# Kernel optimization log

Hardware: AMD Instinct MI355X
Metric: run time of the kernel (lower is better)

## Reference

```python
import jax, jax.numpy as jnp
import numpy as np

AVG_STEP_WEIGHTING = 0.002


def _mean_rbf_kernel(a, b):
    """Mean over all (i,j) of exp(-||a_i - b_j||^2 / 2), features flattened.

    Equivalent to the original per-row loop: (1/N) * sum_i mean_j k(b, a_i).
    Uses the Gram trick to avoid materializing (N, M, D) intermediates.
    """
    A = a.reshape(a.shape[0], -1)  # (N, D)
    B = b.reshape(b.shape[0], -1)  # (M, D)
    sq_a = jnp.sum(A * A, axis=1)  # (N,)
    sq_b = jnp.sum(B * B, axis=1)  # (M,)
    # (N, M) pairwise squared distances; clamp tiny negatives from fp error
    d2 = jnp.maximum(sq_a[:, None] + sq_b[None, :] - 2.0 * (A @ B.T), 0.0)
    return jnp.mean(jnp.exp(-0.5 * d2))


def setup_inputs() -> dict:
    key = jax.random.key(0)
    kx, ky = jax.random.split(key)
    N, M, D1, D2 = 4096, 4096, 24, 8
    x = jax.random.normal(kx, (N, D1, D2), dtype=jnp.float32)
    y = jax.random.normal(ky, (M, D1, D2), dtype=jnp.float32)
    avg_step = jnp.asarray(5.0, dtype=jnp.float32)
    return {"x": x, "y": y, "avg_step": avg_step}


def reference(x, y, avg_step):
    XX = _mean_rbf_kernel(x, x)
    XY = _mean_rbf_kernel(x, y)
    YY = _mean_rbf_kernel(y, y)
    mmd = XX + YY - 2.0 * XY
    loss = mmd + (jnp.maximum(jnp.asarray(1.0, x.dtype), avg_step) - 1.0) * AVG_STEP_WEIGHTING
    return (loss, mmd)
```

## Files before the change

kernel.cpp:

```cpp
#include <hip/hip_runtime.h>
#include <hip/hip_bf16.h>

typedef __attribute__((ext_vector_type(8))) short short8;
typedef __attribute__((ext_vector_type(4))) float float4v;

#define N_ROWS 4096
#define K_DIM  192
#define TILE   128
#define NT     32
#define NSYM   528
#define NBLK   2080
#define LDSS   104
#define C1     (-0.72134752044448179f)
#define LOG2E  (1.4426950408889634f)

__global__ void prep_kernel(const float* __restrict__ x, const float* __restrict__ y,
                            __hip_bfloat16* __restrict__ xb, __hip_bfloat16* __restrict__ yb,
                            float* __restrict__ sqx, float* __restrict__ sqy)
{
    int w    = (blockIdx.x * blockDim.x + threadIdx.x) >> 6;
    int lane = threadIdx.x & 63;
    if (w >= 2 * N_ROWS) return;
    const float*      src = (w < N_ROWS) ? (x + (size_t)w * K_DIM) : (y + (size_t)(w - N_ROWS) * K_DIM);
    __hip_bfloat16*   dst = (w < N_ROWS) ? (xb + (size_t)w * K_DIM) : (yb + (size_t)(w - N_ROWS) * K_DIM);
    float s = 0.f;
    #pragma unroll
    for (int i = 0; i < 3; ++i) {
        float f = src[lane + 64 * i];
        __hip_bfloat16 h = __float2bfloat16(f);
        dst[lane + 64 * i] = h;
        float fb = __bfloat162float(h);
        s += fb * fb;
    }
    #pragma unroll
    for (int off = 32; off; off >>= 1) s += __shfl_down(s, off, 64);
    if (lane == 0) {
        if (w < N_ROWS) sqx[w] = s; else sqy[w - N_ROWS] = s;
    }
}

__global__ void gram_kernel(const __hip_bfloat16* __restrict__ xb, const __hip_bfloat16* __restrict__ yb,
                            const float* __restrict__ sqx, const float* __restrict__ sqy,
                            float* __restrict__ partials)
{
    __shared__ short lA[TILE * LDSS];
    __shared__ short lB[TILE * LDSS];
    __shared__ float wred[4];

    const short* xbs = (const short*)xb;
    const short* ybs = (const short*)yb;

    int id = blockIdx.x;
    const short *A, *B; const float *sa, *sb;
    int bi, bj;
    float weight = 1.0f;
    if (id < 2 * NSYM) {
        int t;
        if (id < NSYM) { t = id;        A = xbs; B = xbs; sa = sqx; sb = sqx; }
        else           { t = id - NSYM; A = ybs; B = ybs; sa = sqy; sb = sqy; }
        bi = 0;
        while (t >= NT - bi) { t -= NT - bi; ++bi; }
        bj = bi + t;
        if (bi != bj) weight = 2.0f;
    } else {
        int t = id - 2 * NSYM;
        bi = t >> 5; bj = t & 31;
        A = xbs; B = ybs; sa = sqx; sb = sqy;
    }
    const int abase = bi * TILE, bbase = bj * TILE;

    const int tid  = threadIdx.x;
    const int lane = tid & 63, w = tid >> 6;
    const int wm   = w >> 1,  wn = w & 1;
    const int m15  = lane & 15, quad = lane >> 4;

    float4v acc[4][4];
    #pragma unroll
    for (int i = 0; i < 4; ++i)
        #pragma unroll
        for (int j = 0; j < 4; ++j) acc[i][j] = (float4v){0.f, 0.f, 0.f, 0.f};

    for (int s = 0; s < 2; ++s) {
        const int k0 = s * 96;
        if (s) __syncthreads();
        #pragma unroll
        for (int it = 0; it < 6; ++it) {
            int c   = it * 256 + tid;
            int row = c / 12;
            int cw  = c - row * 12;
            uint4 va = *(const uint4*)(A + ((size_t)(abase + row) * K_DIM + k0 + cw * 8));
            uint4 vb = *(const uint4*)(B + ((size_t)(bbase + row) * K_DIM + k0 + cw * 8));
            *(uint4*)((char*)lA + row * (LDSS * 2) + cw * 16) = va;
            *(uint4*)((char*)lB + row * (LDSS * 2) + cw * 16) = vb;
        }
        __syncthreads();
        #pragma unroll
        for (int ks = 0; ks < 3; ++ks) {
            short8 af[4], bfr[4];
            const int colb = (ks * 32 + quad * 8) * 2;
            #pragma unroll
            for (int tm = 0; tm < 4; ++tm)
                af[tm] = *(const short8*)((const char*)lA + (wm * 64 + tm * 16 + m15) * (LDSS * 2) + colb);
            #pragma unroll
            for (int tn = 0; tn < 4; ++tn)
                bfr[tn] = *(const short8*)((const char*)lB + (wn * 64 + tn * 16 + m15) * (LDSS * 2) + colb);
            #pragma unroll
            for (int tm = 0; tm < 4; ++tm)
                #pragma unroll
                for (int tn = 0; tn < 4; ++tn)
                    acc[tm][tn] = __builtin_amdgcn_mfma_f32_16x16x32_bf16(af[tm], bfr[tn], acc[tm][tn], 0, 0, 0);
        }
    }

    float u[16], v[4];
    #pragma unroll
    for (int tm = 0; tm < 4; ++tm)
        #pragma unroll
        for (int r = 0; r < 4; ++r)
            u[tm * 4 + r] = C1 * sa[abase + wm * 64 + tm * 16 + quad * 4 + r];
    #pragma unroll
    for (int tn = 0; tn < 4; ++tn)
        v[tn] = C1 * sb[bbase + wn * 64 + tn * 16 + m15];

    float lsum = 0.f;
    #pragma unroll
    for (int tm = 0; tm < 4; ++tm)
        #pragma unroll
        for (int tn = 0; tn < 4; ++tn)
            #pragma unroll
            for (int r = 0; r < 4; ++r) {
                float g  = acc[tm][tn][r];
                float sv = fminf(u[tm * 4 + r] + v[tn] + LOG2E * g, 0.f);
                lsum += exp2f(sv);
            }

    #pragma unroll
    for (int off = 32; off; off >>= 1) lsum += __shfl_down(lsum, off, 64);
    if (lane == 0) wred[w] = lsum;
    __syncthreads();
    if (tid == 0) partials[id] = weight * (wred[0] + wred[1] + wred[2] + wred[3]);
}

__global__ void final_kernel(const float* __restrict__ partials, const float* __restrict__ avg_step,
                             float* __restrict__ out)
{
    __shared__ float red[3][4];
    int tid = threadIdx.x, lane = tid & 63, w = tid >> 6;
    float s0 = 0.f, s1 = 0.f, s2 = 0.f;
    for (int i = tid; i < NSYM; i += 256) s0 += partials[i];
    for (int i = tid; i < NSYM; i += 256) s1 += partials[NSYM + i];
    for (int i = tid; i < 1024; i += 256) s2 += partials[2 * NSYM + i];
    #pragma unroll
    for (int off = 32; off; off >>= 1) {
        s0 += __shfl_down(s0, off, 64);
        s1 += __shfl_down(s1, off, 64);
        s2 += __shfl_down(s2, off, 64);
    }
    if (lane == 0) { red[0][w] = s0; red[1][w] = s1; red[2][w] = s2; }
    __syncthreads();
    if (tid == 0) {
        float sxx = red[0][0] + red[0][1] + red[0][2] + red[0][3];
        float syy = red[1][0] + red[1][1] + red[1][2] + red[1][3];
        float sxy = red[2][0] + red[2][1] + red[2][2] + red[2][3];
        const float inv = 1.0f / 16777216.0f;
        float XX = sxx * inv, YY = syy * inv, XY = sxy * inv;
        float mmd  = XX + YY - 2.0f * XY;
        float stepv = fmaxf(1.0f, avg_step[0]);
        float loss = mmd + (stepv - 1.0f) * 0.002f;
        out[0] = loss;
        out[1] = mmd;
    }
}

extern "C" void kernel_launch(void* const* d_in, const int* in_sizes, int n_in,
                              void* d_out, int out_size, void* d_ws, size_t ws_size,
                              hipStream_t stream)
{
    const float* x        = (const float*)d_in[0];
    const float* y        = (const float*)d_in[1];
    const float* avg_step = (const float*)d_in[2];

    char* ws = (char*)d_ws;
    __hip_bfloat16* xb       = (__hip_bfloat16*)(ws);
    __hip_bfloat16* yb       = (__hip_bfloat16*)(ws + 1572864);
    float*          sqx      = (float*)(ws + 3145728);
    float*          sqy      = (float*)(ws + 3162112);
    float*          partials = (float*)(ws + 3178496);

    prep_kernel<<<2048, 256, 0, stream>>>(x, y, xb, yb, sqx, sqy);
    gram_kernel<<<NBLK, 256, 0, stream>>>(xb, yb, sqx, sqy, partials);
    final_kernel<<<1, 256, 0, stream>>>(partials, avg_step, (float*)d_out);
}
```

Measured before the change: 94.08 us.

## Double-buffer gram tiles via direct global-to-LDS loads with XOR swizzle

Replaces the two-stage register-staged LDS fill with a six-step K loop (32 columns per step) using global_load_lds into a double-buffered, XOR-swizzled LDS layout, so loads of the next K slice overlap MFMA work on the current one. The padded LDS rows give way to a swizzle to avoid bank conflicts, and the total LDS footprint shrinks. The prep kernel is also vectorized to float4 loads and packed bf16 stores. The cost is more barriers, and correctness depends on the swizzle and per-wave LDS addressing of the direct-to-LDS loads matching the fragment reads.

```diff
diff --git a/kernel.cpp b/kernel.cpp
--- a/kernel.cpp
+++ b/kernel.cpp
@@ -3,6 +3,7 @@
 
 typedef __attribute__((ext_vector_type(8))) short short8;
 typedef __attribute__((ext_vector_type(4))) float float4v;
+typedef __attribute__((ext_vector_type(4))) short short4v;
 
 #define N_ROWS 4096
 #define K_DIM  192
@@ -10,9 +11,15 @@
 #define NT     32
 #define NSYM   528
 #define NBLK   2080
-#define LDSS   104
 #define C1     (-0.72134752044448179f)
 #define LOG2E  (1.4426950408889634f)
+
+__device__ __forceinline__ void gl16(const short* g, short* l)
+{
+    __builtin_amdgcn_global_load_lds((const __attribute__((address_space(1))) void*)g,
+                                     (__attribute__((address_space(3))) void*)l,
+                                     16, 0, 0);
+}
 
 __global__ void prep_kernel(const float* __restrict__ x, const float* __restrict__ y,
                             __hip_bfloat16* __restrict__ xb, __hip_bfloat16* __restrict__ yb,
@@ -21,16 +28,21 @@
     int w    = (blockIdx.x * blockDim.x + threadIdx.x) >> 6;
     int lane = threadIdx.x & 63;
     if (w >= 2 * N_ROWS) return;
-    const float*      src = (w < N_ROWS) ? (x + (size_t)w * K_DIM) : (y + (size_t)(w - N_ROWS) * K_DIM);
-    __hip_bfloat16*   dst = (w < N_ROWS) ? (xb + (size_t)w * K_DIM) : (yb + (size_t)(w - N_ROWS) * K_DIM);
+    const float* src = (w < N_ROWS) ? (x + (size_t)w * K_DIM) : (y + (size_t)(w - N_ROWS) * K_DIM);
+    short*       dst = (short*)((w < N_ROWS) ? (xb + (size_t)w * K_DIM)
+                                             : (yb + (size_t)(w - N_ROWS) * K_DIM));
     float s = 0.f;
-    #pragma unroll
-    for (int i = 0; i < 3; ++i) {
-        float f = src[lane + 64 * i];
-        __hip_bfloat16 h = __float2bfloat16(f);
-        dst[lane + 64 * i] = h;
-        float fb = __bfloat162float(h);
-        s += fb * fb;
+    if (lane < 48) {
+        float4v v = *(const float4v*)(src + lane * 4);
+        short4v h;
+        #pragma unroll
+        for (int i = 0; i < 4; ++i) {
+            __hip_bfloat16 b = __float2bfloat16(v[i]);
+            h[i] = *(short*)&b;
+            float fb = __bfloat162float(b);
+            s += fb * fb;
+        }
+        *(short4v*)(dst + lane * 4) = h;
     }
     #pragma unroll
     for (int off = 32; off; off >>= 1) s += __shfl_down(s, off, 64);
@@ -39,12 +51,12 @@
     }
 }
 
-__global__ void gram_kernel(const __hip_bfloat16* __restrict__ xb, const __hip_bfloat16* __restrict__ yb,
+__global__ __launch_bounds__(256) void gram_kernel(const __hip_bfloat16* __restrict__ xb,
+                            const __hip_bfloat16* __restrict__ yb,
                             const float* __restrict__ sqx, const float* __restrict__ sqy,
                             float* __restrict__ partials)
 {
-    __shared__ short lA[TILE * LDSS];
-    __shared__ short lB[TILE * LDSS];
+    __shared__ short lds[16384];
     __shared__ float wred[4];
 
     const short* xbs = (const short*)xb;
@@ -74,43 +86,62 @@
     const int wm   = w >> 1,  wn = w & 1;
     const int m15  = lane & 15, quad = lane >> 4;
 
+    const int crow = tid >> 2;
+    const int xch  = (tid & 3) ^ (crow & 3);
+    const short* srcA = A + (size_t)(abase + crow) * K_DIM + xch * 8;
+    const short* srcB = B + (size_t)(bbase + crow) * K_DIM + xch * 8;
+
+    const int slotq = ((quad ^ (m15 & 3)) * 8);
+    int aoff[4], boff[4];
+    #pragma unroll
+    for (int tm = 0; tm < 4; ++tm) aoff[tm] = (wm * 64 + tm * 16 + m15) * 32 + slotq;
+    #pragma unroll
+    for (int tn = 0; tn < 4; ++tn) boff[tn] = (wn * 64 + tn * 16 + m15) * 32 + slotq;
+
     float4v acc[4][4];
     #pragma unroll
     for (int i = 0; i < 4; ++i)
         #pragma unroll
         for (int j = 0; j < 4; ++j) acc[i][j] = (float4v){0.f, 0.f, 0.f, 0.f};
 
-    for (int s = 0; s < 2; ++s) {
-        const int k0 = s * 96;
-        if (s) __syncthreads();
-        #pragma unroll
-        for (int it = 0; it < 6; ++it) {
-            int c   = it * 256 + tid;
-            int row = c / 12;
-            int cw  = c - row * 12;
-            uint4 va = *(const uint4*)(A + ((size_t)(abase + row) * K_DIM + k0 + cw * 8));
-            uint4 vb = *(const uint4*)(B + ((size_t)(bbase + row) * K_DIM + k0 + cw * 8));
-            *(uint4*)((char*)lA + row * (LDSS * 2) + cw * 16) = va;
-            *(uint4*)((char*)lB + row * (LDSS * 2) + cw * 16) = vb;
-        }
+#define STAGE(p, k0)                                                         \
+    {                                                                        \
+        short* da = lds + (p) * 8192 + (tid & 0xC0) * 8;        \
+        gl16(srcA + (k0),               da);               \
+        gl16(srcA + (k0) + 64 * K_DIM,  da + 2048);        \
+        short* db = da + 4096;                                               \
+        gl16(srcB + (k0),               db);                                 \
+        gl16(srcB + (k0) + 64 * K_DIM,  db + 2048);                          \
+    }
+
+#define COMPUTE(p)                                                           \
+    {                                                                        \
+        const short* a0 = lds + (p) * 8192;                                  \
+        const short* b0 = a0 + 4096;                                         \
+        short8 af[4], bfr[4];                                                \
+        _Pragma("unroll")                                                    \
+        for (int tm = 0; tm < 4; ++tm) af[tm]  = *(const short8*)(a0 + aoff[tm]); \
+        _Pragma("unroll")                                                    \
+        for (int tn = 0; tn < 4; ++tn) bfr[tn] = *(const short8*)(b0 + boff[tn]); \
+        _Pragma("unroll")                                                    \
+        for (int tm = 0; tm < 4; ++tm)                                       \
+            _Pragma("unroll")                                                \
+            for (int tn = 0; tn < 4; ++tn)                                   \
+                acc[tm][tn] = __builtin_amdgcn_mfma_f32_16x16x32_bf16(af[tm], bfr[tn], acc[tm][tn], 0, 0, 0); \
+    }
+
+    STAGE(0, 0)
+    __syncthreads();
+    #pragma unroll
+    for (int s = 1; s <= 5; ++s) {
+        STAGE(s & 1, s * 32)
+        COMPUTE((s - 1) & 1)
         __syncthreads();
-        #pragma unroll
-        for (int ks = 0; ks < 3; ++ks) {
-            short8 af[4], bfr[4];
-            const int colb = (ks * 32 + quad * 8) * 2;
-            #pragma unroll
-            for (int tm = 0; tm < 4; ++tm)
-                af[tm] = *(const short8*)((const char*)lA + (wm * 64 + tm * 16 + m15) * (LDSS * 2) + colb);
-            #pragma unroll
-            for (int tn = 0; tn < 4; ++tn)
-                bfr[tn] = *(const short8*)((const char*)lB + (wn * 64 + tn * 16 + m15) * (LDSS * 2) + colb);
-            #pragma unroll
-            for (int tm = 0; tm < 4; ++tm)
-                #pragma unroll
-                for (int tn = 0; tn < 4; ++tn)
-                    acc[tm][tn] = __builtin_amdgcn_mfma_f32_16x16x32_bf16(af[tm], bfr[tn], acc[tm][tn], 0, 0, 0);
-        }
-    }
+    }
+    COMPUTE(1)
+
+#undef STAGE
+#undef COMPUTE
 
     float u[16], v[4];
     #pragma unroll
```

Result: faster. 90.80 us (-3.5%).
